# Performance work log

Hardware: AMD Instinct MI355X
Metric: run time of the kernel (lower is better)

## Reference

```python
import jax, jax.numpy as jnp
import numpy as np
from jax import lax

DN = ('NCHW', 'OIHW', 'NCHW')
EPS = 1e-5


def conv2d(x, w, b, pad):
    y = lax.conv_general_dilated(x, w, (1, 1), [(pad, pad), (pad, pad)], dimension_numbers=DN)
    return y + b[None, :, None, None]


def setup_inputs() -> dict:
    B, C, G, O, H, W = 2, 64, 64, 64, 256, 256
    key = jax.random.key(0)
    ks = jax.random.split(key, 12)
    s = 0.05
    return {
        'input': jax.random.normal(ks[0], (B, C, H, W), jnp.float32),
        'guidance': jax.random.normal(ks[1], (B, G, H, W), jnp.float32),
        # channel-wise kernel-generating network (two 3x3 convs)
        'cw_w1': jax.random.normal(ks[2], (C, C + G, 3, 3), jnp.float32) * s,
        'cw_b1': jnp.zeros((C,), jnp.float32),
        'cw_w2': jax.random.normal(ks[3], (9 * C, C, 3, 3), jnp.float32) * s,
        'cw_b2': jnp.zeros((9 * C,), jnp.float32),
        # depth-wise kernel-generating network (3x3 conv -> GAP -> 1x1 conv)
        'dw_w1': jax.random.normal(ks[4], (C, C + G, 3, 3), jnp.float32) * s,
        'dw_b1': jnp.zeros((C,), jnp.float32),
        'dw_w2': jax.random.normal(ks[5], (C * O, C, 1, 1), jnp.float32) * s,
        'dw_b2': jnp.zeros((C * O,), jnp.float32),
        # BatchNorm affine params
        'bn_gamma': jnp.ones((O,), jnp.float32),
        'bn_beta': jnp.zeros((O,), jnp.float32),
    }


def reference(input, guidance, cw_w1, cw_b1, cw_w2, cw_b2,
              dw_w1, dw_b1, dw_w2, dw_b2, bn_gamma, bn_beta):
    B, C, H, W = input.shape
    kgn_in = jnp.concatenate((input, guidance), axis=1)

    # channel-wise per-pixel 3x3 weights: [B, 9C, H, W]
    cw = conv2d(jax.nn.relu(conv2d(kgn_in, cw_w1, cw_b1, 1)), cw_w2, cw_b2, 1)

    # depth-wise per-sample 1x1 weights: [B, C*O, 1, 1]
    h = jax.nn.relu(conv2d(kgn_in, dw_w1, dw_b1, 1))
    h = jnp.mean(h, axis=(2, 3), keepdims=True)  # AdaptiveAvgPool2d((1,1))
    dw = conv2d(h, dw_w2, dw_b2, 0)
    O = dw.shape[1] // C

    # guided separable conv: spatially-varying depthwise 3x3 then per-sample 1x1
    # patches ordered (C, kh, kw) channel-major -> [B, C, 9, H, W]
    patches = lax.conv_general_dilated_patches(
        input, filter_shape=(3, 3), window_strides=(1, 1), padding='SAME',
        dimension_numbers=DN).reshape(B, C, 9, H, W)
    cw = cw.reshape(B, C, 9, H, W)
    y = jnp.sum(patches * cw, axis=2)  # [B, C, H, W]

    dw = dw.reshape(B, O, C)
    z = jnp.einsum('bchw,boc->bohw', y, dw)  # per-sample 1x1 conv

    # BatchNorm2d (training-mode batch stats) + ReLU
    mu = jnp.mean(z, axis=(0, 2, 3), keepdims=True)
    var = jnp.var(z, axis=(0, 2, 3), keepdims=True)
    zn = (z - mu) * lax.rsqrt(var + EPS)
    out = jax.nn.relu(zn * bn_gamma[None, :, None, None] + bn_beta[None, :, None, None])
    return out
```

## Files before the change

### kernel.cpp

```cpp
#include <hip/hip_runtime.h>

typedef short v8s __attribute__((ext_vector_type(8)));
typedef float v4f __attribute__((ext_vector_type(4)));

__device__ inline unsigned short f2bf(float f) {
    unsigned u = __float_as_uint(f);
    u += 0x7fff + ((u >> 16) & 1);
    return (unsigned short)(u >> 16);
}
__device__ inline float bf2f(unsigned short h) {
    return __uint_as_float(((unsigned)h) << 16);
}

__device__ inline void gload_lds16(const void* g, void* l) {
    __builtin_amdgcn_global_load_lds(
        (const __attribute__((address_space(1))) unsigned*)(unsigned long long)(uintptr_t)g,
        (__attribute__((address_space(3))) unsigned*)(unsigned)(uintptr_t)l, 16, 0, 0);
}

__global__ void transpose_kernel(const float* __restrict__ input, const float* __restrict__ guidance,
                                 char* __restrict__ X0, char* __restrict__ inN)
{
    const int r = blockIdx.x, b = blockIdx.y, px = threadIdx.x;
    const size_t hw = (size_t)r * 256 + px;
    char* xrow = X0 + (((size_t)b * 65536 + hw) << 8);
    char* irow = inN + (((size_t)b * 65536 + hw) << 7);
    const int rot = (px & 7) << 4;
    for (int c8 = 0; c8 < 16; ++c8) {
        unsigned sh[4];
#pragma unroll
        for (int e = 0; e < 8; e += 2) {
            int c0 = c8 * 8 + e;
            float f0 = (c0 < 64) ? input[(((size_t)(b * 64 + c0)) << 16) + hw]
                                 : guidance[(((size_t)(b * 64 + c0 - 64)) << 16) + hw];
            float f1 = (c0 + 1 < 64) ? input[(((size_t)(b * 64 + c0 + 1)) << 16) + hw]
                                     : guidance[(((size_t)(b * 64 + c0 - 63)) << 16) + hw];
            sh[e >> 1] = (unsigned)f2bf(f0) | ((unsigned)f2bf(f1) << 16);
        }
        uint4 pk = make_uint4(sh[0], sh[1], sh[2], sh[3]);
        *(uint4*)(xrow + ((c8 * 16 + rot) & 255)) = pk;
        if (c8 < 8) *(uint4*)(irow + ((c8 * 16 + rot) & 127)) = pk;
    }
}

__global__ void prepack1_kernel(const float* __restrict__ w1, const float* __restrict__ w2,
                                char* __restrict__ d1, char* __restrict__ d2)
{
    const float* src = blockIdx.y ? w2 : w1;
    char* dst = blockIdx.y ? d2 : d1;
    int t = blockIdx.x * 256 + threadIdx.x;
    int jj = t & 7, lane = (t >> 3) & 63;
    int r2 = t >> 9;
    int ng = r2 & 3, r3 = r2 >> 2;
    int ick = r3 & 3, tau = r3 >> 2;
    if (tau >= 9) return;
    int n  = ng * 16 + (lane & 15);
    int ic = ick * 32 + (lane >> 4) * 8 + jj;
    float v = src[(((size_t)n * 128 + ic) * 3 + tau / 3) * 3 + tau % 3];
    *(unsigned short*)(dst + (size_t)t * 2) = f2bf(v);
}

__global__ void prepack2_kernel(const float* __restrict__ src, char* __restrict__ dst)
{
    int t = blockIdx.x * 256 + threadIdx.x;
    int jj = t & 7, lane = (t >> 3) & 63;
    int r2 = t >> 9;
    int ng = r2 % 36, r3 = r2 / 36;
    int ick = r3 & 1, tau = r3 >> 1;
    if (tau >= 9) return;
    int n  = ng * 16 + (lane & 15);
    int ic = ick * 32 + (lane >> 4) * 8 + jj;
    int oc = (n & 63) * 9 + (n >> 6);
    float v = src[(((size_t)oc * 64 + ic) * 3 + tau / 3) * 3 + tau % 3];
    *(unsigned short*)(dst + (size_t)t * 2) = f2bf(v);
}

__global__ __launch_bounds__(256, 2) void conv1_mfma(
    const char* __restrict__ X0, const char* __restrict__ Bp1, const char* __restrict__ Bp2,
    const float* __restrict__ b1, const float* __restrict__ b2,
    char* __restrict__ t1, float* __restrict__ hsum)
{
    constexpr int PP = 66 * 256;
    __shared__ __align__(16) char As[3 * PP];
    __shared__ __align__(16) char Bs[4 * 4096];

    const int tid = threadIdx.x, lane = tid & 63, w = tid >> 6;
    const int m16 = lane & 15, q = lane >> 4;
    const int col0 = blockIdx.x * 64;
    const int row  = blockIdx.y;
    const int b    = blockIdx.z;

    const char* rowbase = X0 + ((size_t)b * 65536) * 256;
    for (int idx = tid; idx < 3 * 1056; idx += 256) {
        int plane = idx / 1056;
        int gr = row + plane - 1;
        if ((unsigned)gr < 256u) {
            int wb  = (idx - plane * 1056) * 16;
            int pxo = wb >> 8;
            int gpx = min(max(col0 - 1 + pxo, 0), 255);
            gload_lds16(rowbase + (((size_t)gr * 256 + gpx) << 8) + (wb & 255),
                        As + (idx & ~63) * 16);
        }
    }
    __syncthreads();
    if (col0 == 0 && tid < 48)
        *(uint4*)(As + (tid / 16) * PP + (tid & 15) * 16) = make_uint4(0, 0, 0, 0);
    if (col0 == 192 && tid < 48)
        *(uint4*)(As + (tid / 16) * PP + 65 * 256 + (tid & 15) * 16) = make_uint4(0, 0, 0, 0);

    v4f acc[4][2];
#pragma unroll
    for (int mg = 0; mg < 4; ++mg) { acc[mg][0] = (v4f)(0.f); acc[mg][1] = (v4f)(0.f); }

    for (int ty = 0; ty < 3; ++ty) {
        int gr = row + ty - 1;
        if ((unsigned)gr >= 256u) continue;
        const char* plane = As + ty * PP;
        for (int tx = 0; tx < 3; ++tx) {
            for (int ick0 = 0; ick0 < 4; ick0 += 2) {
                const int kstep = (ty * 3 + tx) * 4 + ick0;
                __syncthreads();
                for (int idx = tid; idx < 1024; idx += 256) {
                    int ii = idx >> 9, set = (idx >> 8) & 1, off16 = idx & 255;
                    const char* src = (set ? Bp2 : Bp1) + (size_t)(kstep + ii) * 4096 + off16 * 16;
                    gload_lds16(src, Bs + (idx & ~63) * 16);
                }
                __syncthreads();
#pragma unroll
                for (int ii = 0; ii < 2; ++ii) {
                    const int ick = ick0 + ii;
                    v8s af[4];
#pragma unroll
                    for (int mg = 0; mg < 4; ++mg) {
                        int px  = col0 + mg * 16 + m16 + tx - 1;
                        int tpx = mg * 16 + m16 + tx;
                        int off = (ick * 64 + q * 16 + ((px & 7) << 4)) & 255;
                        af[mg] = *(const v8s*)(plane + tpx * 256 + off);
                    }
#pragma unroll
                    for (int set = 0; set < 2; ++set) {
                        v8s bf = *(const v8s*)(Bs + ((ii * 2 + set) << 12) + (w << 10) + (lane << 4));
#pragma unroll
                        for (int mg = 0; mg < 4; ++mg)
                            acc[mg][set] = __builtin_amdgcn_mfma_f32_16x16x32_bf16(af[mg], bf, acc[mg][set], 0, 0, 0);
                    }
                }
            }
        }
    }

    const int oc = w * 16 + m16;
    {
        float bb = b1[oc];
        char* dst = t1 + (((size_t)(b * 256 + row)) << 8) * 128;
#pragma unroll
        for (int mg = 0; mg < 4; ++mg)
#pragma unroll
            for (int r = 0; r < 4; ++r) {
                int px = col0 + mg * 16 + (q << 2) + r;
                float v = fmaxf(acc[mg][0][r] + bb, 0.f);
                *(unsigned short*)(dst + (size_t)px * 128 + ((oc * 2 + ((px & 7) << 4)) & 127)) = f2bf(v);
            }
    }
    {
        float bb = b2[oc];
        float s = 0.f;
#pragma unroll
        for (int mg = 0; mg < 4; ++mg)
#pragma unroll
            for (int r = 0; r < 4; ++r) s += fmaxf(acc[mg][1][r] + bb, 0.f);
        s += __shfl_xor(s, 16, 64);
        s += __shfl_xor(s, 32, 64);
        if (lane < 16) atomicAdd(&hsum[b * 64 + oc], s);
    }
}

__global__ void dw_gemm_kernel(const float* __restrict__ hsum, const float* __restrict__ w2,
                               const float* __restrict__ b2, float* __restrict__ dwout)
{
    __shared__ float h[64];
    int idx = blockIdx.x * 256 + threadIdx.x;
    int b = idx >> 12, n = idx & 4095;
    if (threadIdx.x < 64) h[threadIdx.x] = hsum[b * 64 + threadIdx.x] * (1.f / 65536.f);
    __syncthreads();
    float a = 0.f;
#pragma unroll
    for (int k = 0; k < 64; ++k) a = fmaf(h[k], w2[(size_t)n * 64 + k], a);
    dwout[idx] = a + b2[n];
}

__global__ void dwprep_kernel(const float* __restrict__ dwbuf, char* __restrict__ dwp)
{
    int t = blockIdx.x * 256 + threadIdx.x;
    int jj = t & 7, lane = (t >> 3) & 63;
    int r = t >> 9;
    int owg = r & 3, kick = (r >> 2) & 1, b = r >> 3;
    int o = owg * 16 + (lane & 15);
    int c = kick * 32 + ((lane >> 4) << 3) + jj;
    *(unsigned short*)(dwp + (size_t)t * 2) = f2bf(dwbuf[b * 4096 + o * 64 + c]);
}

__global__ __launch_bounds__(256, 2) void conv2yz_kernel(
    const char* __restrict__ t1, const char* __restrict__ inN,
    const char* __restrict__ Bp2, const char* __restrict__ dwp,
    const float* __restrict__ cw_b2, float* __restrict__ zout)
{
    constexpr int PPA = 66 * 128;
    constexpr int BSZ = 36864;
    __shared__ __align__(16) char pool[70400];
    char* Bs = pool;
    char* As = pool + 36864;
    char* Dw = pool + 62208;
    char* Pt = pool;
    char* Ys = pool + 25344;

    const int tid = threadIdx.x, lane = tid & 63, w = tid >> 6;
    const int m16 = lane & 15, q = lane >> 4;
    const int col0 = blockIdx.x * 64;
    const int row  = blockIdx.y;
    const int b    = blockIdx.z;
    const int c_lane = w * 16 + m16;

    float bias9[9];
#pragma unroll
    for (int j = 0; j < 9; ++j) bias9[j] = cw_b2[c_lane * 9 + j];

    for (int idx = tid; idx < 512; idx += 256)
        gload_lds16(dwp + (size_t)b * 8192 + idx * 16, Dw + (idx & ~63) * 16);

    const char* rowbase = t1 + ((size_t)b * 65536) * 128;
    for (int idx = tid; idx < 3 * 528; idx += 256) {
        int plane = idx / 528;
        int gr = row + plane - 1;
        if ((unsigned)gr < 256u) {
            int wb  = (idx - plane * 528) * 16;
            int pxo = wb >> 7;
            int gpx = min(max(col0 - 1 + pxo, 0), 255);
            gload_lds16(rowbase + (((size_t)gr * 256 + gpx) << 7) + (wb & 127),
                        As + (idx & ~63) * 16);
        }
    }
    __syncthreads();
    if (col0 == 0 && tid < 24)
        *(uint4*)(As + (tid / 8) * PPA + (tid & 7) * 16) = make_uint4(0, 0, 0, 0);
    if (col0 == 192 && tid < 24)
        *(uint4*)(As + (tid / 8) * PPA + 65 * 128 + (tid & 7) * 16) = make_uint4(0, 0, 0, 0);

    v4f acc[4][9];
#pragma unroll
    for (int mg = 0; mg < 4; ++mg)
#pragma unroll
        for (int ng = 0; ng < 9; ++ng) acc[mg][ng] = (v4f)(0.f);

    for (int ty = 0; ty < 3; ++ty) {
        int gr = row + ty - 1;
        if ((unsigned)gr >= 256u) continue;
        const char* plane = As + ty * PPA;
        for (int tx = 0; tx < 3; ++tx) {
            for (int ick = 0; ick < 2; ++ick) {
                __syncthreads();
                const char* bsrc = Bp2 + (size_t)((ty * 3 + tx) * 2 + ick) * BSZ;
                for (int idx = tid; idx < 2304; idx += 256)
                    gload_lds16(bsrc + idx * 16, Bs + (idx & ~63) * 16);
                __syncthreads();
                v8s af[4];
#pragma unroll
                for (int mg = 0; mg < 4; ++mg) {
                    int px  = col0 + mg * 16 + m16 + tx - 1;
                    int tpx = mg * 16 + m16 + tx;
                    int off = (ick * 64 + q * 16 + ((px & 7) << 4)) & 127;
                    af[mg] = *(const v8s*)(plane + tpx * 128 + off);
                }
#pragma unroll
                for (int ng = 0; ng < 9; ++ng) {
                    v8s bf = *(const v8s*)(Bs + (((ng << 2) + w) << 10) + (lane << 4));
#pragma unroll
                    for (int mg = 0; mg < 4; ++mg)
                        acc[mg][ng] = __builtin_amdgcn_mfma_f32_16x16x32_bf16(af[mg], bf, acc[mg][ng], 0, 0, 0);
                }
            }
        }
    }

    __syncthreads();
    const char* prow = inN + ((size_t)b * 65536) * 128;
    for (int idx = tid; idx < 3 * 528; idx += 256) {
        int plane = idx / 528;
        int gr = row + plane - 1;
        if ((unsigned)gr < 256u) {
            int wb  = (idx - plane * 528) * 16;
            int pxo = wb >> 7;
            int gpx = min(max(col0 - 1 + pxo, 0), 255);
            gload_lds16(prow + (((size_t)gr * 256 + gpx) << 7) + (wb & 127),
                        Pt + (idx & ~63) * 16);
        }
    }
    __syncthreads();
    if (col0 == 0 && tid < 24)
        *(uint4*)(Pt + (tid / 8) * PPA + (tid & 7) * 16) = make_uint4(0, 0, 0, 0);
    if (col0 == 192 && tid < 24)
        *(uint4*)(Pt + (tid / 8) * PPA + 65 * 128 + (tid & 7) * 16) = make_uint4(0, 0, 0, 0);
    __syncthreads();

    float yv[4][4];
#pragma unroll
    for (int mg = 0; mg < 4; ++mg)
#pragma unroll
        for (int r = 0; r < 4; ++r) yv[mg][r] = 0.f;

    for (int jy = 0; jy < 3; ++jy) {
        if ((unsigned)(row + jy - 1) >= 256u) continue;
        const char* pp = Pt + jy * PPA;
        for (int jx = 0; jx < 3; ++jx) {
            const int j = jy * 3 + jx;
            const float bj = bias9[j];
#pragma unroll
            for (int mg = 0; mg < 4; ++mg)
#pragma unroll
                for (int r = 0; r < 4; ++r) {
                    int tpx = mg * 16 + (q << 2) + r + jx;
                    unsigned short pv = *(const unsigned short*)
                        (pp + tpx * 128 + ((c_lane * 2 + (((tpx - 1) & 7) << 4)) & 127));
                    yv[mg][r] = fmaf(acc[mg][j][r] + bj, bf2f(pv), yv[mg][r]);
                }
        }
    }

#pragma unroll
    for (int mg = 0; mg < 4; ++mg)
#pragma unroll
        for (int r = 0; r < 4; ++r) {
            int px_t = mg * 16 + (q << 2) + r;
            *(unsigned short*)(Ys + px_t * 128 + ((c_lane * 2 + ((px_t & 7) << 4)) & 127)) = f2bf(yv[mg][r]);
        }
    __syncthreads();

    v4f zacc[4];
#pragma unroll
    for (int mg = 0; mg < 4; ++mg) zacc[mg] = (v4f)(0.f);
#pragma unroll
    for (int kick = 0; kick < 2; ++kick) {
        v8s bf = *(const v8s*)(Dw + (((kick << 2) + w) << 10) + (lane << 4));
#pragma unroll
        for (int mg2 = 0; mg2 < 4; ++mg2) {
            int off = ((kick << 6) + (q << 4) + ((m16 & 7) << 4)) & 127;
            v8s af2 = *(const v8s*)(Ys + (mg2 * 16 + m16) * 128 + off);
            zacc[mg2] = __builtin_amdgcn_mfma_f32_16x16x32_bf16(af2, bf, zacc[mg2], 0, 0, 0);
        }
    }

    const int o = w * 16 + m16;
    float* zp = zout + (((size_t)(b * 64 + o)) << 16) + ((size_t)row << 8);
#pragma unroll
    for (int mg2 = 0; mg2 < 4; ++mg2) {
        float4 vv = make_float4(zacc[mg2][0], zacc[mg2][1], zacc[mg2][2], zacc[mg2][3]);
        *(float4*)(zp + col0 + mg2 * 16 + (q << 2)) = vv;
    }
}

__global__ void stats_kernel(const float* __restrict__ z, float* __restrict__ s1, float* __restrict__ s2)
{
    int o = blockIdx.x, ch = blockIdx.y;
    float a1 = 0.f, a2 = 0.f;
    for (int t = threadIdx.x; t < 8192; t += 256) {
        float v0 = z[((size_t)o << 16) + (ch << 13) + t];
        float v1 = z[((size_t)(64 + o) << 16) + (ch << 13) + t];
        a1 += v0 + v1;
        a2 += v0 * v0 + v1 * v1;
    }
#pragma unroll
    for (int d = 32; d > 0; d >>= 1) { a1 += __shfl_xor(a1, d, 64); a2 += __shfl_xor(a2, d, 64); }
    __shared__ float r1[4], r2[4];
    int w = threadIdx.x >> 6;
    if ((threadIdx.x & 63) == 0) { r1[w] = a1; r2[w] = a2; }
    __syncthreads();
    if (threadIdx.x == 0) {
        atomicAdd(&s1[o], r1[0] + r1[1] + r1[2] + r1[3]);
        atomicAdd(&s2[o], r2[0] + r2[1] + r2[2] + r2[3]);
    }
}

__global__ void bn_kernel(const float* __restrict__ z, const float* __restrict__ s1,
                          const float* __restrict__ s2, const float* __restrict__ gamma,
                          const float* __restrict__ beta, float* __restrict__ outp)
{
    size_t idx = ((size_t)blockIdx.x * 256 + threadIdx.x) * 4;
    int o = (int)((idx >> 16) & 63);
    float mu  = s1[o] * (1.f / 131072.f);
    float var = s2[o] * (1.f / 131072.f) - mu * mu;
    float rs  = rsqrtf(var + 1e-5f);
    float scale = gamma[o] * rs;
    float shift = beta[o] - mu * scale;
    float4 v = *(const float4*)(z + idx);
    v.x = fmaxf(v.x * scale + shift, 0.f);
    v.y = fmaxf(v.y * scale + shift, 0.f);
    v.z = fmaxf(v.z * scale + shift, 0.f);
    v.w = fmaxf(v.w * scale + shift, 0.f);
    *(float4*)(outp + idx) = v;
}

extern "C" void kernel_launch(void* const* d_in, const int* in_sizes, int n_in,
                              void* d_out, int out_size, void* d_ws, size_t ws_size,
                              hipStream_t stream)
{
    const float* input    = (const float*)d_in[0];
    const float* guidance = (const float*)d_in[1];
    const float* cw_w1    = (const float*)d_in[2];
    const float* cw_b1    = (const float*)d_in[3];
    const float* cw_w2    = (const float*)d_in[4];
    const float* cw_b2    = (const float*)d_in[5];
    const float* dw_w1    = (const float*)d_in[6];
    const float* dw_b1    = (const float*)d_in[7];
    const float* dw_w2    = (const float*)d_in[8];
    const float* dw_b2    = (const float*)d_in[9];
    const float* gamma    = (const float*)d_in[10];
    const float* beta     = (const float*)d_in[11];

    char* ws = (char*)d_ws;
    char*  inN   = ws;
    char*  t1    = ws + 16777216;
    char*  Bp1   = ws + 33554432;
    char*  Bpdw  = ws + 33701888;
    char*  Bp2   = ws + 33849344;
    float* hsum  = (float*)(ws + 34512896);
    float* s1    = (float*)(ws + 34513408);
    float* s2    = (float*)(ws + 34513664);
    float* dwbuf = (float*)(ws + 34513920);
    char*  dwp   = ws + 34546688;

    char* X0 = (char*)d_out;

    hipMemsetAsync(hsum, 0, 1024, stream);

    transpose_kernel<<<dim3(256, 2), 256, 0, stream>>>(input, guidance, X0, inN);
    prepack1_kernel<<<dim3(288, 2), 256, 0, stream>>>(cw_w1, dw_w1, Bp1, Bpdw);
    prepack2_kernel<<<1296, 256, 0, stream>>>(cw_w2, Bp2);

    conv1_mfma<<<dim3(4, 256, 2), 256, 0, stream>>>(X0, Bp1, Bpdw, cw_b1, dw_b1, t1, hsum);
    dw_gemm_kernel<<<32, 256, 0, stream>>>(hsum, dw_w2, dw_b2, dwbuf);
    dwprep_kernel<<<32, 256, 0, stream>>>(dwbuf, dwp);

    conv2yz_kernel<<<dim3(4, 256, 2), 256, 0, stream>>>(t1, inN, Bp2, dwp, cw_b2, (float*)d_out);

    stats_kernel<<<dim3(64, 8), 256, 0, stream>>>((const float*)d_out, s1, s2);
    bn_kernel<<<8192, 256, 0, stream>>>((const float*)d_out, s1, s2, gamma, beta, (float*)d_out);
}
```

Measured before the change: 395.9 us.

## Read conv weights directly from global, merge small kernels, LDS-transpose input

The conv1 and conv2 MFMA loops now read packed B fragments straight from global memory (cached) instead of staging them in LDS behind per-step barriers. This removes many __syncthreads and frees LDS, so conv1 raises its occupancy bound to 3. The transpose kernel now goes through an LDS tile so global writes are coalesced. The three prepack kernels merge into one launch, as do dw_gemm and dwprep. conv2 also loads the t1 and input tiles together up front. The cost is global or L2 latency on the B loads inside the MFMA loop, which the higher occupancy is meant to hide.

```diff
diff --git a/kernel.cpp b/kernel.cpp
--- a/kernel.cpp
+++ b/kernel.cpp
@@ -21,68 +21,86 @@
 __global__ void transpose_kernel(const float* __restrict__ input, const float* __restrict__ guidance,
                                  char* __restrict__ X0, char* __restrict__ inN)
 {
-    const int r = blockIdx.x, b = blockIdx.y, px = threadIdx.x;
-    const size_t hw = (size_t)r * 256 + px;
-    char* xrow = X0 + (((size_t)b * 65536 + hw) << 8);
-    char* irow = inN + (((size_t)b * 65536 + hw) << 7);
-    const int rot = (px & 7) << 4;
-    for (int c8 = 0; c8 < 16; ++c8) {
-        unsigned sh[4];
-#pragma unroll
-        for (int e = 0; e < 8; e += 2) {
-            int c0 = c8 * 8 + e;
-            float f0 = (c0 < 64) ? input[(((size_t)(b * 64 + c0)) << 16) + hw]
-                                 : guidance[(((size_t)(b * 64 + c0 - 64)) << 16) + hw];
-            float f1 = (c0 + 1 < 64) ? input[(((size_t)(b * 64 + c0 + 1)) << 16) + hw]
-                                     : guidance[(((size_t)(b * 64 + c0 - 63)) << 16) + hw];
-            sh[e >> 1] = (unsigned)f2bf(f0) | ((unsigned)f2bf(f1) << 16);
-        }
-        uint4 pk = make_uint4(sh[0], sh[1], sh[2], sh[3]);
-        *(uint4*)(xrow + ((c8 * 16 + rot) & 255)) = pk;
-        if (c8 < 8) *(uint4*)(irow + ((c8 * 16 + rot) & 127)) = pk;
-    }
-}
-
-__global__ void prepack1_kernel(const float* __restrict__ w1, const float* __restrict__ w2,
-                                char* __restrict__ d1, char* __restrict__ d2)
-{
-    const float* src = blockIdx.y ? w2 : w1;
-    char* dst = blockIdx.y ? d2 : d1;
-    int t = blockIdx.x * 256 + threadIdx.x;
-    int jj = t & 7, lane = (t >> 3) & 63;
-    int r2 = t >> 9;
-    int ng = r2 & 3, r3 = r2 >> 2;
-    int ick = r3 & 3, tau = r3 >> 2;
-    if (tau >= 9) return;
-    int n  = ng * 16 + (lane & 15);
-    int ic = ick * 32 + (lane >> 4) * 8 + jj;
-    float v = src[(((size_t)n * 128 + ic) * 3 + tau / 3) * 3 + tau % 3];
-    *(unsigned short*)(dst + (size_t)t * 2) = f2bf(v);
-}
-
-__global__ void prepack2_kernel(const float* __restrict__ src, char* __restrict__ dst)
-{
-    int t = blockIdx.x * 256 + threadIdx.x;
-    int jj = t & 7, lane = (t >> 3) & 63;
-    int r2 = t >> 9;
-    int ng = r2 % 36, r3 = r2 / 36;
-    int ick = r3 & 1, tau = r3 >> 1;
-    if (tau >= 9) return;
-    int n  = ng * 16 + (lane & 15);
-    int ic = ick * 32 + (lane >> 4) * 8 + jj;
-    int oc = (n & 63) * 9 + (n >> 6);
-    float v = src[(((size_t)oc * 64 + ic) * 3 + tau / 3) * 3 + tau % 3];
-    *(unsigned short*)(dst + (size_t)t * 2) = f2bf(v);
-}
-
-__global__ __launch_bounds__(256, 2) void conv1_mfma(
+    __shared__ unsigned lds[64 * 66];
+    const int tid = threadIdx.x;
+    const int b = blockIdx.y;
+    const size_t hw0 = (size_t)blockIdx.x * 64;
+
+    for (int it = 0; it < 16; ++it) {
+        int p  = it * 4 + (tid >> 6);
+        int px = tid & 63;
+        size_t hw = hw0 + px;
+        int c0 = 2 * p;
+        float f0 = (c0 < 64) ? input[((size_t)(b * 64 + c0) << 16) + hw]
+                             : guidance[((size_t)(b * 64 + c0 - 64) << 16) + hw];
+        float f1 = (c0 + 1 < 64) ? input[((size_t)(b * 64 + c0 + 1) << 16) + hw]
+                                 : guidance[((size_t)(b * 64 + c0 - 63) << 16) + hw];
+        lds[px * 66 + p] = (unsigned)f2bf(f0) | ((unsigned)f2bf(f1) << 16);
+    }
+    __syncthreads();
+
+    char* xbase = X0 + (((size_t)b * 65536 + hw0) << 8);
+    for (int it = 0; it < 4; ++it) {
+        int chunk = it * 256 + tid;
+        int px  = chunk >> 4;
+        int ofs = (chunk & 15) << 4;
+        int u   = (ofs - ((px & 7) << 4)) & 255;
+        const unsigned* s = &lds[px * 66 + (u >> 2)];
+        *(uint4*)(xbase + px * 256 + ofs) = make_uint4(s[0], s[1], s[2], s[3]);
+    }
+    char* ibase = inN + (((size_t)b * 65536 + hw0) << 7);
+    for (int it = 0; it < 2; ++it) {
+        int chunk = it * 256 + tid;
+        int px  = chunk >> 3;
+        int ofs = (chunk & 7) << 4;
+        int u   = (ofs - ((px & 7) << 4)) & 127;
+        const unsigned* s = &lds[px * 66 + (u >> 2)];
+        *(uint4*)(ibase + px * 128 + ofs) = make_uint4(s[0], s[1], s[2], s[3]);
+    }
+}
+
+__global__ void prepack_all(const float* __restrict__ cw_w2, const float* __restrict__ cw_w1,
+                            const float* __restrict__ dw_w1, char* __restrict__ Bp2,
+                            char* __restrict__ Bp1, char* __restrict__ Bpdw)
+{
+    int bid = blockIdx.x;
+    if (bid < 1296) {
+        int t = bid * 256 + threadIdx.x;
+        int jj = t & 7, lane = (t >> 3) & 63;
+        int r2 = t >> 9;
+        int ng = r2 % 36, r3 = r2 / 36;
+        int ick = r3 & 1, tau = r3 >> 1;
+        if (tau >= 9) return;
+        int n  = ng * 16 + (lane & 15);
+        int ic = ick * 32 + (lane >> 4) * 8 + jj;
+        int oc = (n & 63) * 9 + (n >> 6);
+        float v = cw_w2[(((size_t)oc * 64 + ic) * 3 + tau / 3) * 3 + tau % 3];
+        *(unsigned short*)(Bp2 + (size_t)t * 2) = f2bf(v);
+    } else {
+        int s = bid - 1296;
+        int set = (s >= 288);
+        const float* src = set ? dw_w1 : cw_w1;
+        char* dst = set ? Bpdw : Bp1;
+        int t = (set ? s - 288 : s) * 256 + threadIdx.x;
+        int jj = t & 7, lane = (t >> 3) & 63;
+        int r2 = t >> 9;
+        int ng = r2 & 3, r3 = r2 >> 2;
+        int ick = r3 & 3, tau = r3 >> 2;
+        if (tau >= 9) return;
+        int n  = ng * 16 + (lane & 15);
+        int ic = ick * 32 + (lane >> 4) * 8 + jj;
+        float v = src[(((size_t)n * 128 + ic) * 3 + tau / 3) * 3 + tau % 3];
+        *(unsigned short*)(dst + (size_t)t * 2) = f2bf(v);
+    }
+}
+
+__global__ __launch_bounds__(256, 3) void conv1_mfma(
     const char* __restrict__ X0, const char* __restrict__ Bp1, const char* __restrict__ Bp2,
     const float* __restrict__ b1, const float* __restrict__ b2,
     char* __restrict__ t1, float* __restrict__ hsum)
 {
     constexpr int PP = 66 * 256;
     __shared__ __align__(16) char As[3 * PP];
-    __shared__ __align__(16) char Bs[4 * 4096];
 
     const int tid = threadIdx.x, lane = tid & 63, w = tid >> 6;
     const int m16 = lane & 15, q = lane >> 4;
@@ -107,44 +125,37 @@
         *(uint4*)(As + (tid / 16) * PP + (tid & 15) * 16) = make_uint4(0, 0, 0, 0);
     if (col0 == 192 && tid < 48)
         *(uint4*)(As + (tid / 16) * PP + 65 * 256 + (tid & 15) * 16) = make_uint4(0, 0, 0, 0);
+    __syncthreads();
 
     v4f acc[4][2];
 #pragma unroll
     for (int mg = 0; mg < 4; ++mg) { acc[mg][0] = (v4f)(0.f); acc[mg][1] = (v4f)(0.f); }
 
+    const int boff = (w << 10) + (lane << 4);
     for (int ty = 0; ty < 3; ++ty) {
         int gr = row + ty - 1;
         if ((unsigned)gr >= 256u) continue;
         const char* plane = As + ty * PP;
         for (int tx = 0; tx < 3; ++tx) {
-            for (int ick0 = 0; ick0 < 4; ick0 += 2) {
-                const int kstep = (ty * 3 + tx) * 4 + ick0;
-                __syncthreads();
-                for (int idx = tid; idx < 1024; idx += 256) {
-                    int ii = idx >> 9, set = (idx >> 8) & 1, off16 = idx & 255;
-                    const char* src = (set ? Bp2 : Bp1) + (size_t)(kstep + ii) * 4096 + off16 * 16;
-                    gload_lds16(src, Bs + (idx & ~63) * 16);
+#pragma unroll
+            for (int ick = 0; ick < 4; ++ick) {
+                const int kstep = (ty * 3 + tx) * 4 + ick;
+                v8s af[4];
+#pragma unroll
+                for (int mg = 0; mg < 4; ++mg) {
+                    int px  = col0 + mg * 16 + m16 + tx - 1;
+                    int tpx = mg * 16 + m16 + tx;
+                    int off = (ick * 64 + q * 16 + ((px & 7) << 4)) & 255;
+                    af[mg] = *(const v8s*)(plane + tpx * 256 + off);
                 }
-                __syncthreads();
-#pragma unroll
-                for (int ii = 0; ii < 2; ++ii) {
-                    const int ick = ick0 + ii;
-                    v8s af[4];
-#pragma unroll
-                    for (int mg = 0; mg < 4; ++mg) {
-                        int px  = col0 + mg * 16 + m16 + tx - 1;
-                        int tpx = mg * 16 + m16 + tx;
-                        int off = (ick * 64 + q * 16 + ((px & 7) << 4)) & 255;
-                        af[mg] = *(const v8s*)(plane + tpx * 256 + off);
-                    }
-#pragma unroll
-                    for (int set = 0; set < 2; ++set) {
-                        v8s bf = *(const v8s*)(Bs + ((ii * 2 + set) << 12) + (w << 10) + (lane << 4));
-#pragma unroll
-                        for (int mg = 0; mg < 4; ++mg)
-                            acc[mg][set] = __builtin_amdgcn_mfma_f32_16x16x32_bf16(af[mg], bf, acc[mg][set], 0, 0, 0);
-                    }
-                }
+                v8s bf0 = *(const v8s*)(Bp1 + (size_t)kstep * 4096 + boff);
+                v8s bf1 = *(const v8s*)(Bp2 + (size_t)kstep * 4096 + boff);
+#pragma unroll
+                for (int mg = 0; mg < 4; ++mg)
+                    acc[mg][0] = __builtin_amdgcn_mfma_f32_16x16x32_bf16(af[mg], bf0, acc[mg][0], 0, 0, 0);
+#pragma unroll
+                for (int mg = 0; mg < 4; ++mg)
+                    acc[mg][1] = __builtin_amdgcn_mfma_f32_16x16x32_bf16(af[mg], bf1, acc[mg][1], 0, 0, 0);
             }
         }
     }
@@ -175,29 +186,24 @@
     }
 }
 
-__global__ void dw_gemm_kernel(const float* __restrict__ hsum, const float* __restrict__ w2,
-                               const float* __restrict__ b2, float* __restrict__ dwout)
+__global__ void dwfused_kernel(const float* __restrict__ hsum, const float* __restrict__ w2,
+                               const float* __restrict__ b2, char* __restrict__ dwp)
 {
     __shared__ float h[64];
-    int idx = blockIdx.x * 256 + threadIdx.x;
-    int b = idx >> 12, n = idx & 4095;
+    int t = blockIdx.x * 256 + threadIdx.x;
+    int b = t >> 12;
     if (threadIdx.x < 64) h[threadIdx.x] = hsum[b * 64 + threadIdx.x] * (1.f / 65536.f);
     __syncthreads();
-    float a = 0.f;
-#pragma unroll
-    for (int k = 0; k < 64; ++k) a = fmaf(h[k], w2[(size_t)n * 64 + k], a);
-    dwout[idx] = a + b2[n];
-}
-
-__global__ void dwprep_kernel(const float* __restrict__ dwbuf, char* __restrict__ dwp)
-{
-    int t = blockIdx.x * 256 + threadIdx.x;
     int jj = t & 7, lane = (t >> 3) & 63;
     int r = t >> 9;
-    int owg = r & 3, kick = (r >> 2) & 1, b = r >> 3;
+    int owg = r & 3, kick = (r >> 2) & 1;
     int o = owg * 16 + (lane & 15);
     int c = kick * 32 + ((lane >> 4) << 3) + jj;
-    *(unsigned short*)(dwp + (size_t)t * 2) = f2bf(dwbuf[b * 4096 + o * 64 + c]);
+    int n = o * 64 + c;
+    float a = 0.f;
+#pragma unroll
+    for (int k = 0; k < 64; ++k) a = fmaf(h[k], w2[(size_t)n * 64 + k], a);
+    *(unsigned short*)(dwp + (size_t)t * 2) = f2bf(a + b2[n]);
 }
 
 __global__ __launch_bounds__(256, 2) void conv2yz_kernel(
@@ -206,13 +212,10 @@
     const float* __restrict__ cw_b2, float* __restrict__ zout)
 {
     constexpr int PPA = 66 * 128;
-    constexpr int BSZ = 36864;
-    __shared__ __align__(16) char pool[70400];
-    char* Bs = pool;
-    char* As = pool + 36864;
-    char* Dw = pool + 62208;
-    char* Pt = pool;
-    char* Ys = pool + 25344;
+    __shared__ __align__(16) char As[3 * PPA];
+    __shared__ __align__(16) char Pt[3 * PPA];
+    __shared__ __align__(16) char Ys[8192];
+    __shared__ __align__(16) char Dw[8192];
 
     const int tid = threadIdx.x, lane = tid & 63, w = tid >> 6;
     const int m16 = lane & 15, q = lane >> 4;
@@ -221,68 +224,9 @@
     const int b    = blockIdx.z;
     const int c_lane = w * 16 + m16;
 
-    float bias9[9];
-#pragma unroll
-    for (int j = 0; j < 9; ++j) bias9[j] = cw_b2[c_lane * 9 + j];
-
     for (int idx = tid; idx < 512; idx += 256)
         gload_lds16(dwp + (size_t)b * 8192 + idx * 16, Dw + (idx & ~63) * 16);
-
-    const char* rowbase = t1 + ((size_t)b * 65536) * 128;
-    for (int idx = tid; idx < 3 * 528; idx += 256) {
-        int plane = idx / 528;
-        int gr = row + plane - 1;
-        if ((unsigned)gr < 256u) {
-            int wb  = (idx - plane * 528) * 16;
-            int pxo = wb >> 7;
-            int gpx = min(max(col0 - 1 + pxo, 0), 255);
-            gload_lds16(rowbase + (((size_t)gr * 256 + gpx) << 7) + (wb & 127),
-                        As + (idx & ~63) * 16);
-        }
-    }
-    __syncthreads();
-    if (col0 == 0 && tid < 24)
-        *(uint4*)(As + (tid / 8) * PPA + (tid & 7) * 16) = make_uint4(0, 0, 0, 0);
-    if (col0 == 192 && tid < 24)
-        *(uint4*)(As + (tid / 8) * PPA + 65 * 128 + (tid & 7) * 16) = make_uint4(0, 0, 0, 0);
-
-    v4f acc[4][9];
-#pragma unroll
-    for (int mg = 0; mg < 4; ++mg)
-#pragma unroll
-        for (int ng = 0; ng < 9; ++ng) acc[mg][ng] = (v4f)(0.f);
-
-    for (int ty = 0; ty < 3; ++ty) {
-        int gr = row + ty - 1;
-        if ((unsigned)gr >= 256u) continue;
-        const char* plane = As + ty * PPA;
-        for (int tx = 0; tx < 3; ++tx) {
-            for (int ick = 0; ick < 2; ++ick) {
-                __syncthreads();
-                const char* bsrc = Bp2 + (size_t)((ty * 3 + tx) * 2 + ick) * BSZ;
-                for (int idx = tid; idx < 2304; idx += 256)
-                    gload_lds16(bsrc + idx * 16, Bs + (idx & ~63) * 16);
-                __syncthreads();
-                v8s af[4];
-#pragma unroll
-                for (int mg = 0; mg < 4; ++mg) {
-                    int px  = col0 + mg * 16 + m16 + tx - 1;
-                    int tpx = mg * 16 + m16 + tx;
-                    int off = (ick * 64 + q * 16 + ((px & 7) << 4)) & 127;
-                    af[mg] = *(const v8s*)(plane + tpx * 128 + off);
-                }
-#pragma unroll
-                for (int ng = 0; ng < 9; ++ng) {
-                    v8s bf = *(const v8s*)(Bs + (((ng << 2) + w) << 10) + (lane << 4));
-#pragma unroll
-                    for (int mg = 0; mg < 4; ++mg)
-                        acc[mg][ng] = __builtin_amdgcn_mfma_f32_16x16x32_bf16(af[mg], bf, acc[mg][ng], 0, 0, 0);
-                }
-            }
-        }
-    }
-
-    __syncthreads();
+    const char* arow = t1  + ((size_t)b * 65536) * 128;
     const char* prow = inN + ((size_t)b * 65536) * 128;
     for (int idx = tid; idx < 3 * 528; idx += 256) {
         int plane = idx / 528;
@@ -291,16 +235,61 @@
             int wb  = (idx - plane * 528) * 16;
             int pxo = wb >> 7;
             int gpx = min(max(col0 - 1 + pxo, 0), 255);
-            gload_lds16(prow + (((size_t)gr * 256 + gpx) << 7) + (wb & 127),
-                        Pt + (idx & ~63) * 16);
-        }
-    }
-    __syncthreads();
-    if (col0 == 0 && tid < 24)
+            size_t goff = (((size_t)gr * 256 + gpx) << 7) + (wb & 127);
+            gload_lds16(arow + goff, As + (idx & ~63) * 16);
+            gload_lds16(prow + goff, Pt + (idx & ~63) * 16);
+        }
+    }
+    __syncthreads();
+    if (col0 == 0 && tid < 24) {
+        *(uint4*)(As + (tid / 8) * PPA + (tid & 7) * 16) = make_uint4(0, 0, 0, 0);
         *(uint4*)(Pt + (tid / 8) * PPA + (tid & 7) * 16) = make_uint4(0, 0, 0, 0);
-    if (col0 == 192 && tid < 24)
+    }
+    if (col0 == 192 && tid < 24) {
+        *(uint4*)(As + (tid / 8) * PPA + 65 * 128 + (tid & 7) * 16) = make_uint4(0, 0, 0, 0);
         *(uint4*)(Pt + (tid / 8) * PPA + 65 * 128 + (tid & 7) * 16) = make_uint4(0, 0, 0, 0);
-    __syncthreads();
+    }
+    __syncthreads();
+
+    float bias9[9];
+#pragma unroll
+    for (int j = 0; j < 9; ++j) bias9[j] = cw_b2[c_lane * 9 + j];
+
+    v4f acc[4][9];
+#pragma unroll
+    for (int mg = 0; mg < 4; ++mg)
+#pragma unroll
+        for (int ng = 0; ng < 9; ++ng) acc[mg][ng] = (v4f)(0.f);
+
+    const int boff = (w << 10) + (lane << 4);
+    for (int ty = 0; ty < 3; ++ty) {
+        int gr = row + ty - 1;
+        if ((unsigned)gr >= 256u) continue;
+        const char* plane = As + ty * PPA;
+#pragma unroll 1
+        for (int tx = 0; tx < 3; ++tx) {
+#pragma unroll
+            for (int ick = 0; ick < 2; ++ick) {
+                const int kstep = (ty * 3 + tx) * 2 + ick;
+                v8s af[4];
+#pragma unroll
+                for (int mg = 0; mg < 4; ++mg) {
+                    int px  = col0 + mg * 16 + m16 + tx - 1;
+                    int tpx = mg * 16 + m16 + tx;
+                    int off = (ick * 64 + q * 16 + ((px & 7) << 4)) & 127;
+                    af[mg] = *(const v8s*)(plane + tpx * 128 + off);
+                }
+                const char* bbase = Bp2 + (size_t)kstep * 36864 + boff;
+#pragma unroll
+                for (int ng = 0; ng < 9; ++ng) {
+                    v8s bf = *(const v8s*)(bbase + (ng << 12));
+#pragma unroll
+                    for (int mg = 0; mg < 4; ++mg)
+                        acc[mg][ng] = __builtin_amdgcn_mfma_f32_16x16x32_bf16(af[mg], bf, acc[mg][ng], 0, 0, 0);
+                }
+            }
+        }
+    }
 
     float yv[4][4];
 #pragma unroll
@@ -425,20 +414,17 @@
     float* hsum  = (float*)(ws + 34512896);
     float* s1    = (float*)(ws + 34513408);
     float* s2    = (float*)(ws + 34513664);
-    float* dwbuf = (float*)(ws + 34513920);
-    char*  dwp   = ws + 34546688;
+    char*  dwp   = ws + 34513920;
 
     char* X0 = (char*)d_out;
 
     hipMemsetAsync(hsum, 0, 1024, stream);
 
-    transpose_kernel<<<dim3(256, 2), 256, 0, stream>>>(input, guidance, X0, inN);
-    prepack1_kernel<<<dim3(288, 2), 256, 0, stream>>>(cw_w1, dw_w1, Bp1, Bpdw);
-    prepack2_kernel<<<1296, 256, 0, stream>>>(cw_w2, Bp2);
+    transpose_kernel<<<dim3(1024, 2), 256, 0, stream>>>(input, guidance, X0, inN);
+    prepack_all<<<1872, 256, 0, stream>>>(cw_w2, cw_w1, dw_w1, Bp2, Bp1, Bpdw);
 
     conv1_mfma<<<dim3(4, 256, 2), 256, 0, stream>>>(X0, Bp1, Bpdw, cw_b1, dw_b1, t1, hsum);
-    dw_gemm_kernel<<<32, 256, 0, stream>>>(hsum, dw_w2, dw_b2, dwbuf);
-    dwprep_kernel<<<32, 256, 0, stream>>>(dwbuf, dwp);
+    dwfused_kernel<<<32, 256, 0, stream>>>(hsum, dw_w2, dw_b2, dwp);
 
     conv2yz_kernel<<<dim3(4, 256, 2), 256, 0, stream>>>(t1, inN, Bp2, dwp, cw_b2, (float*)d_out);
 
```

After: 324.3 us. 1.22x faster.
